# Kernel optimization log

Hardware: AMD Instinct MI355X
Metric: run time of the kernel (lower is better)

The kernel has to match this reference:

```python
import jax, jax.numpy as jnp
import numpy as np

DIMS = [784, 256, 128, 64, 32, 10]
PCT = [0.5, 0.1, 0.5, 0.5]          # KWinners percent_on per layer
KS = [128, 13, 32, 16]              # k = round(n * percent_on)
BOOST = 1.4
SPARSITY = 0.1                      # fraction of weights kept nonzero
BATCH = 65536


def setup_inputs() -> dict:
    key = jax.random.key(0)
    ks = jax.random.split(key, 16)
    inp = {"x": jax.random.normal(ks[0], (BATCH, 784), jnp.float32)}
    for i in range(5):
        fan_in = DIMS[i]
        bound = 1.0 / np.sqrt(fan_in)
        w = jax.random.uniform(ks[1 + 2 * i], (DIMS[i + 1], DIMS[i]), jnp.float32, -bound, bound)
        b = jax.random.uniform(ks[2 + 2 * i], (DIMS[i + 1],), jnp.float32, -bound, bound)
        if i < 4:
            mask = (jax.random.uniform(ks[11 + i], (DIMS[i + 1], DIMS[i])) < SPARSITY).astype(jnp.float32)
            w = w * mask
        inp[f"w{i + 1}"] = w
        inp[f"b{i + 1}"] = b
    for i in range(4):  # duty cycles (buffers driving boosting)
        inp[f"duty{i + 1}"] = jax.random.uniform(
            jax.random.fold_in(key, 100 + i), (DIMS[i + 1],), jnp.float32, 0.0, 2.0 * PCT[i])
    return inp


def kwinners(x, duty, percent_on, k):
    # boost = exp(boost_strength * (target_density - duty_cycle))
    boosted = x * jnp.exp(BOOST * (percent_on - duty))
    # per-row k-th largest boosted value as threshold; winners keep raw x
    thresh = jax.lax.top_k(boosted, k)[0][:, -1:]
    return jnp.where(boosted >= thresh, x, jnp.zeros_like(x))


def reference(x, w1, b1, w2, b2, w3, b3, w4, b4, w5, b5, duty1, duty2, duty3, duty4):
    h = x.reshape(x.shape[0], -1)
    h = kwinners(h @ w1.T + b1, duty1, PCT[0], KS[0])
    h = kwinners(h @ w2.T + b2, duty2, PCT[1], KS[1])
    h = kwinners(h @ w3.T + b3, duty3, PCT[2], KS[2])
    h = kwinners(h @ w4.T + b4, duty4, PCT[3], KS[3])
    return h @ w5.T + b5
```

## Files before the change

kernel.cpp:

```cpp
#include <hip/hip_runtime.h>
#include <cstdint>
#include <cstddef>
#include <math.h>

#define NT 512
#define TROWS 64
#define HS 68

typedef __attribute__((ext_vector_type(8))) short bf16x8;
typedef __attribute__((ext_vector_type(4))) float f32x4;

#define WSP2_OFF 614400
#define WSP3_OFF 712704
#define WSP4_OFF 737280

__device__ __forceinline__ uint32_t f2u(float f) {
  uint32_t b = __float_as_uint(f);
  return (b & 0x80000000u) ? ~b : (b | 0x80000000u);
}

__device__ __forceinline__ unsigned short f2bf(float f) {
  uint32_t u = __float_as_uint(f);
  return (unsigned short)((u + 0x7FFFu + ((u >> 16) & 1u)) >> 16);
}
__device__ __forceinline__ float bf2f(unsigned short h) {
  return __uint_as_float(((uint32_t)h) << 16);
}

__device__ __forceinline__ void gload_lds16(const void* g, void* l) {
  __builtin_amdgcn_global_load_lds(
      (const __attribute__((address_space(1))) unsigned int*)g,
      (__attribute__((address_space(3))) unsigned int*)l, 16, 0, 0);
}

__global__ void prep_w1_kernel(const float* __restrict__ w1,
                               unsigned short* __restrict__ wsp) {
  const int idx = blockIdx.x * 256 + threadIdx.x;
  if (idx >= 256 * 800) return;
  const int col = idx / 800, k = idx % 800;
  const float v = (k < 784) ? w1[col * 784 + k] : 0.0f;
  const unsigned short h = f2bf(v);
  const float r1 = v - bf2f(h);
  const unsigned short m = f2bf(r1);
  const float r2 = r1 - bf2f(m);
  const unsigned short l = f2bf(r2);
  const int c = k >> 5, kin = k & 31, kg = kin >> 3, k8 = kin & 7;
  const int tile = col >> 4, c16 = col & 15;
  const size_t base =
      ((size_t)(c * 3) * 16 + tile) * 512 + (size_t)(kg * 16 + c16) * 8 + k8;
  wsp[base]            = h;
  wsp[base + 16 * 512] = m;
  wsp[base + 32 * 512] = l;
}

__global__ void prep_w2_kernel(const float* __restrict__ w2,
                               unsigned short* __restrict__ wsp) {
  const int idx = blockIdx.x * 256 + threadIdx.x;
  if (idx >= 128 * 256) return;
  const int col = idx / 256, k = idx % 256;
  const float v = w2[col * 256 + k];
  const unsigned short h = f2bf(v);
  const float r1 = v - bf2f(h);
  const unsigned short m = f2bf(r1);
  const float r2 = r1 - bf2f(m);
  const unsigned short l = f2bf(r2);
  const int c2 = k >> 5, kin = k & 31, kg = kin >> 3, k8 = kin & 7;
  const int tile = col >> 4, c16 = col & 15;
  unsigned short* w2p = wsp + WSP2_OFF;
  const size_t base =
      ((size_t)(c2 * 3) * 8 + tile) * 512 + (size_t)(kg * 16 + c16) * 8 + k8;
  w2p[base]            = h;
  w2p[base + 8 * 512]  = m;
  w2p[base + 16 * 512] = l;
}

__global__ void prep_w3_kernel(const float* __restrict__ w3,
                               unsigned short* __restrict__ wsp) {
  const int idx = blockIdx.x * 256 + threadIdx.x;
  if (idx >= 64 * 128) return;
  const int col = idx / 128, k = idx % 128;
  const float v = w3[col * 128 + k];
  const unsigned short h = f2bf(v);
  const float r1 = v - bf2f(h);
  const unsigned short m = f2bf(r1);
  const float r2 = r1 - bf2f(m);
  const unsigned short l = f2bf(r2);
  const int c3 = k >> 5, kin = k & 31, kg = kin >> 3, k8 = kin & 7;
  const int tile = col >> 4, c16 = col & 15;
  unsigned short* w3p = wsp + WSP3_OFF;
  const size_t base =
      ((size_t)(c3 * 3) * 4 + tile) * 512 + (size_t)(kg * 16 + c16) * 8 + k8;
  w3p[base]            = h;
  w3p[base + 4 * 512]  = m;
  w3p[base + 8 * 512]  = l;
}

__global__ void prep_w4_kernel(const float* __restrict__ w4,
                               unsigned short* __restrict__ wsp) {
  const int idx = blockIdx.x * 256 + threadIdx.x;
  if (idx >= 32 * 64) return;
  const int col = idx / 64, k = idx % 64;
  const float v = w4[col * 64 + k];
  const unsigned short h = f2bf(v);
  const float r1 = v - bf2f(h);
  const unsigned short m = f2bf(r1);
  const float r2 = r1 - bf2f(m);
  const unsigned short l = f2bf(r2);
  const int c4 = k >> 5, kin = k & 31, kg = kin >> 3, k8 = kin & 7;
  const int tile = col >> 4, c16 = col & 15;
  unsigned short* w4p = wsp + WSP4_OFF;
  const size_t base =
      ((size_t)(c4 * 3) * 2 + tile) * 512 + (size_t)(kg * 16 + c16) * 8 + k8;
  w4p[base]            = h;
  w4p[base + 2 * 512]  = m;
  w4p[base + 4 * 512]  = l;
}

template<int NCOL, int K>
__device__ __forceinline__ void kwinners_inplace(
    float* __restrict__ ht, const float* __restrict__ duty,
    float pct, int wid, int lane)
{
  constexpr int Q = (NCOL + 63) / 64;
  const bool active = (NCOL >= 64) || (lane < NCOL);
  float Bq[Q];
#pragma unroll
  for (int q = 0; q < Q; ++q) {
    const int col = active ? (lane + 64 * q) : 0;
    const float arg = 1.4f * (pct - duty[col]);
    Bq[q] = (float)exp((double)arg);
  }
#pragma unroll
  for (int g = 0; g < 2; ++g) {
    const int r0 = wid * 8 + g * 4;
    float h[Q][4];
    uint32_t u[Q][4];
#pragma unroll
    for (int q = 0; q < Q; ++q) {
      const int col = active ? (lane + 64 * q) : 0;
      *(float4*)&h[q][0] = *(const float4*)&ht[col * HS + r0];
#pragma unroll
      for (int m = 0; m < 4; ++m)
        u[q][m] = active ? f2u(h[q][m] * Bq[q]) : 0u;
    }
    uint32_t prefix[4] = {0u, 0u, 0u, 0u};
    int done = 0;
    for (int bit = 31; bit >= 0 && done != 15; --bit) {
#pragma unroll
      for (int m = 0; m < 4; ++m) {
        if (done & (1 << m)) continue;
        const uint32_t cand = prefix[m] | (1u << bit);
        int cnt = 0;
#pragma unroll
        for (int q = 0; q < Q; ++q)
          cnt += __popcll(__ballot(u[q][m] >= cand));
        if (cnt >= K) {
          prefix[m] = cand;
          if (cnt == K) done |= (1 << m);
        }
      }
    }
#pragma unroll
    for (int m = 0; m < 4; ++m)
#pragma unroll
      for (int q = 0; q < Q; ++q)
        h[q][m] = (u[q][m] >= prefix[m]) ? h[q][m] : 0.0f;
#pragma unroll
    for (int q = 0; q < Q; ++q) {
      const int col = lane + 64 * q;
      if (active) *(float4*)&ht[col * HS + r0] = *(const float4*)&h[q][0];
    }
  }
}

#define SPLIT3(a8, Ah, Am, Al)                                   \
  _Pragma("unroll")                                              \
  for (int j = 0; j < 8; ++j) {                                  \
    const uint32_t u0 = __float_as_uint(a8[j]);                  \
    Ah[j] = (short)(u0 >> 16);                                   \
    const float r1 = a8[j] - __uint_as_float(u0 & 0xFFFF0000u);  \
    const uint32_t u1 = __float_as_uint(r1);                     \
    Am[j] = (short)(u1 >> 16);                                   \
    const float r2 = r1 - __uint_as_float(u1 & 0xFFFF0000u);     \
    Al[j] = (short)(__float_as_uint(r2) >> 16);                  \
  }

#define MFMA6(ACC, Ah, Am, Al, PB, PSTRIDE)                                  \
  {                                                                          \
    bf16x8 B_ = *(const bf16x8*)(PB);                                        \
    ACC = __builtin_amdgcn_mfma_f32_16x16x32_bf16(Ah, B_, ACC, 0, 0, 0);     \
    ACC = __builtin_amdgcn_mfma_f32_16x16x32_bf16(Am, B_, ACC, 0, 0, 0);     \
    ACC = __builtin_amdgcn_mfma_f32_16x16x32_bf16(Al, B_, ACC, 0, 0, 0);     \
    B_ = *(const bf16x8*)((PB) + (PSTRIDE));                                 \
    ACC = __builtin_amdgcn_mfma_f32_16x16x32_bf16(Ah, B_, ACC, 0, 0, 0);     \
    ACC = __builtin_amdgcn_mfma_f32_16x16x32_bf16(Am, B_, ACC, 0, 0, 0);     \
    B_ = *(const bf16x8*)((PB) + 2 * (PSTRIDE));                             \
    ACC = __builtin_amdgcn_mfma_f32_16x16x32_bf16(Ah, B_, ACC, 0, 0, 0);     \
  }

__global__ __launch_bounds__(NT, 4)
void sparse_fcnet_kernel(
    const float* __restrict__ x,
    const unsigned short* __restrict__ wsp,
    const float* __restrict__ b1, const float* __restrict__ b2,
    const float* __restrict__ b3, const float* __restrict__ b4,
    const float* __restrict__ w5, const float* __restrict__ b5,
    const float* __restrict__ duty1, const float* __restrict__ duty2,
    const float* __restrict__ duty3, const float* __restrict__ duty4,
    float* __restrict__ out)
{
  __shared__ float ht[256 * HS];
  __shared__ float stg[2592];

  const int tid  = threadIdx.x;
  const int lane = tid & 63;
  const int wid  = tid >> 6;
  const int R0   = blockIdx.x * TROWS;

  const int rt  = wid & 3;
  const int ch  = wid >> 2;
  const int l15 = lane & 15;
  const int kg  = lane >> 4;

  {
    unsigned short* wp = (unsigned short*)ht;

    f32x4 acc[8];
#pragma unroll
    for (int t = 0; t < 8; ++t) acc[t] = 0.0f;

    const size_t xrow = (size_t)(R0 + rt * 16 + l15) * 784;
    float xc[8];
    {
      const float4 va = *(const float4*)&x[xrow + kg * 8];
      const float4 vb = *(const float4*)&x[xrow + kg * 8 + 4];
      xc[0]=va.x; xc[1]=va.y; xc[2]=va.z; xc[3]=va.w;
      xc[4]=vb.x; xc[5]=vb.y; xc[6]=vb.z; xc[7]=vb.w;
    }

    for (int c = 0; c < 25; ++c) {
      __syncthreads();
      {
        const unsigned short* wc = wsp + (size_t)c * 24576;
#pragma unroll
        for (int u = 0; u < 6; ++u) {
          const int ubase = (u * 512 + wid * 64) * 8;
          gload_lds16(wc + ubase + lane * 8, &wp[ubase]);
        }
      }
      bf16x8 Ah, Am, Al;
      SPLIT3(xc, Ah, Am, Al)
      if (c < 24) {
        const int kn = (c + 1) * 32 + kg * 8;
        if (kn < 784) {
          const float4 va = *(const float4*)&x[xrow + kn];
          const float4 vb = *(const float4*)&x[xrow + kn + 4];
          xc[0]=va.x; xc[1]=va.y; xc[2]=va.z; xc[3]=va.w;
          xc[4]=vb.x; xc[5]=vb.y; xc[6]=vb.z; xc[7]=vb.w;
        } else {
#pragma unroll
          for (int j = 0; j < 8; ++j) xc[j] = 0.0f;
        }
      }
      __syncthreads();

#pragma unroll
      for (int t = 0; t < 8; ++t) {
        const unsigned short* pb = (const unsigned short*)&wp[(ch * 8 + t) * 512 + lane * 8];
        MFMA6(acc[t], Ah, Am, Al, pb, 8192)
      }
    }
    __syncthreads();

#pragma unroll
    for (int t = 0; t < 8; ++t) {
      const int col_g = ch * 128 + t * 16 + l15;
      const float bv = b1[col_g];
      float4 v = {acc[t].x + bv, acc[t].y + bv, acc[t].z + bv, acc[t].w + bv};
      *(float4*)&ht[col_g * HS + rt * 16 + kg * 4] = v;
    }
  }
  __syncthreads();
  kwinners_inplace<256, 128>(ht, duty1, 0.5f, wid, lane);
  __syncthreads();

  {
    const unsigned short* wsp2 = wsp + WSP2_OFF;
    f32x4 acc2[4];
#pragma unroll
    for (int t = 0; t < 4; ++t) acc2[t] = 0.0f;

    for (int c2 = 0; c2 < 8; ++c2) {
      float a8[8];
#pragma unroll
      for (int j = 0; j < 8; ++j)
        a8[j] = ht[(c2 * 32 + kg * 8 + j) * HS + rt * 16 + l15];
      bf16x8 Ah, Am, Al;
      SPLIT3(a8, Ah, Am, Al)
      const unsigned short* wc2 =
          wsp2 + (size_t)(c2 * 3) * 4096 + (size_t)(ch * 4) * 512 + lane * 8;
#pragma unroll
      for (int t = 0; t < 4; ++t) {
        const unsigned short* pb = wc2 + t * 512;
        MFMA6(acc2[t], Ah, Am, Al, pb, 4096)
      }
    }
    __syncthreads();
#pragma unroll
    for (int t = 0; t < 4; ++t) {
      const int col_g = ch * 64 + t * 16 + l15;
      const float bv = b2[col_g];
      float4 v = {acc2[t].x + bv, acc2[t].y + bv, acc2[t].z + bv, acc2[t].w + bv};
      *(float4*)&ht[col_g * HS + rt * 16 + kg * 4] = v;
    }
  }
  __syncthreads();
  kwinners_inplace<128, 13>(ht, duty2, 0.1f, wid, lane);
  __syncthreads();

  {
    const unsigned short* wsp3 = wsp + WSP3_OFF;
    f32x4 acc3[2];
    acc3[0] = 0.0f; acc3[1] = 0.0f;

    for (int c3 = 0; c3 < 4; ++c3) {
      float a8[8];
#pragma unroll
      for (int j = 0; j < 8; ++j)
        a8[j] = ht[(c3 * 32 + kg * 8 + j) * HS + rt * 16 + l15];
      bf16x8 Ah, Am, Al;
      SPLIT3(a8, Ah, Am, Al)
      const unsigned short* wc3 =
          wsp3 + (size_t)(c3 * 3) * 2048 + (size_t)(ch * 2) * 512 + lane * 8;
#pragma unroll
      for (int t = 0; t < 2; ++t) {
        const unsigned short* pb = wc3 + t * 512;
        MFMA6(acc3[t], Ah, Am, Al, pb, 2048)
      }
    }
    __syncthreads();
#pragma unroll
    for (int t = 0; t < 2; ++t) {
      const int col_g = ch * 32 + t * 16 + l15;
      const float bv = b3[col_g];
      float4 v = {acc3[t].x + bv, acc3[t].y + bv, acc3[t].z + bv, acc3[t].w + bv};
      *(float4*)&ht[col_g * HS + rt * 16 + kg * 4] = v;
    }
  }
  __syncthreads();
  kwinners_inplace<64, 32>(ht, duty3, 0.5f, wid, lane);
  __syncthreads();

  {
    const unsigned short* wsp4 = wsp + WSP4_OFF;
    f32x4 acc4;
    acc4 = 0.0f;

    for (int c4 = 0; c4 < 2; ++c4) {
      float a8[8];
#pragma unroll
      for (int j = 0; j < 8; ++j)
        a8[j] = ht[(c4 * 32 + kg * 8 + j) * HS + rt * 16 + l15];
      bf16x8 Ah, Am, Al;
      SPLIT3(a8, Ah, Am, Al)
      const unsigned short* pb =
          wsp4 + (size_t)(c4 * 3) * 1024 + (size_t)ch * 512 + lane * 8;
      MFMA6(acc4, Ah, Am, Al, pb, 1024)
    }
    __syncthreads();
    {
      const int col_g = ch * 16 + l15;
      const float bv = b4[col_g];
      float4 v = {acc4.x + bv, acc4.y + bv, acc4.z + bv, acc4.w + bv};
      *(float4*)&ht[col_g * HS + rt * 16 + kg * 4] = v;
    }
  }
  __syncthreads();
  kwinners_inplace<32, 16>(ht, duty4, 0.5f, wid, lane);
  __syncthreads();

  {
    if (tid < 320) stg[tid] = w5[tid];
    if (tid < 10)  stg[320 + tid] = b5[tid];
    __syncthreads();
    for (int o = tid; o < 640; o += NT) {
      const int row = o / 10, col = o % 10;
      float acc = 0.0f;
#pragma unroll
      for (int kk = 0; kk < 32; ++kk)
        acc = fmaf(ht[kk * HS + row], stg[col * 32 + kk], acc);
      out[(size_t)(R0 + row) * 10 + col] = acc + stg[320 + col];
    }
  }
}

extern "C" void kernel_launch(void* const* d_in, const int* in_sizes, int n_in,
                              void* d_out, int out_size, void* d_ws, size_t ws_size,
                              hipStream_t stream) {
  const float* x     = (const float*)d_in[0];
  const float* w1    = (const float*)d_in[1];
  const float* b1    = (const float*)d_in[2];
  const float* w2    = (const float*)d_in[3];
  const float* b2    = (const float*)d_in[4];
  const float* w3    = (const float*)d_in[5];
  const float* b3    = (const float*)d_in[6];
  const float* w4    = (const float*)d_in[7];
  const float* b4    = (const float*)d_in[8];
  const float* w5    = (const float*)d_in[9];
  const float* b5    = (const float*)d_in[10];
  const float* duty1 = (const float*)d_in[11];
  const float* duty2 = (const float*)d_in[12];
  const float* duty3 = (const float*)d_in[13];
  const float* duty4 = (const float*)d_in[14];
  float* out = (float*)d_out;
  unsigned short* wsp = (unsigned short*)d_ws;

  hipLaunchKernelGGL(prep_w1_kernel, dim3(800), dim3(256), 0, stream, w1, wsp);
  hipLaunchKernelGGL(prep_w2_kernel, dim3(128), dim3(256), 0, stream, w2, wsp);
  hipLaunchKernelGGL(prep_w3_kernel, dim3(32),  dim3(256), 0, stream, w3, wsp);
  hipLaunchKernelGGL(prep_w4_kernel, dim3(8),   dim3(256), 0, stream, w4, wsp);

  const int rows = in_sizes[0] / 784;
  const int grid = rows / TROWS;
  hipLaunchKernelGGL(sparse_fcnet_kernel, dim3(grid), dim3(NT), 0, stream,
                     x, wsp, b1, b2, b3, b4, w5, b5,
                     duty1, duty2, duty3, duty4, out);
}
```

Baseline: 227.6 us.

## Double-buffer layer-1 weight chunks in LDS and read low-precision part from global

The layer-1 GEMM now prefetches the next weight chunk into a second LDS buffer while computing on the current one. This removes one of the two barriers per chunk iteration. Only the high and mid bf16 weight planes (4 of 6 units) are staged through LDS. The low plane is read directly from global memory, with a register prefetch one tile ahead. This lowers LDS footprint and traffic, but adds global loads inside the MFMA loop and relies on the LDS region being large enough for two 16384-element buffers.

Result: slower. 252.4 us (+10.9%).

```diff
diff --git a/kernel.cpp b/kernel.cpp
--- a/kernel.cpp
+++ b/kernel.cpp
@@ -238,14 +238,25 @@
       xc[4]=vb.x; xc[5]=vb.y; xc[6]=vb.z; xc[7]=vb.w;
     }
 
+    {
+      const unsigned short* wc = wsp;
+#pragma unroll
+      for (int u = 0; u < 4; ++u) {
+        const int ubase = (u * 512 + wid * 64) * 8;
+        gload_lds16(wc + ubase + lane * 8, &wp[ubase]);
+      }
+    }
+    __syncthreads();
+
     for (int c = 0; c < 25; ++c) {
-      __syncthreads();
-      {
-        const unsigned short* wc = wsp + (size_t)c * 24576;
-#pragma unroll
-        for (int u = 0; u < 6; ++u) {
+      unsigned short* cur = wp + (c & 1) * 16384;
+      unsigned short* nxt = wp + ((c + 1) & 1) * 16384;
+      if (c < 24) {
+        const unsigned short* wc = wsp + (size_t)(c + 1) * 24576;
+#pragma unroll
+        for (int u = 0; u < 4; ++u) {
           const int ubase = (u * 512 + wid * 64) * 8;
-          gload_lds16(wc + ubase + lane * 8, &wp[ubase]);
+          gload_lds16(wc + ubase + lane * 8, &nxt[ubase]);
         }
       }
       bf16x8 Ah, Am, Al;
@@ -262,15 +273,28 @@
           for (int j = 0; j < 8; ++j) xc[j] = 0.0f;
         }
       }
+
+      const unsigned short* wl =
+          wsp + (size_t)c * 24576 + 16384 + (size_t)(ch * 8) * 512 + lane * 8;
+      bf16x8 Bl = *(const bf16x8*)(wl);
+
+#pragma unroll
+      for (int t = 0; t < 8; ++t) {
+        bf16x8 Bln;
+        if (t < 7) Bln = *(const bf16x8*)(wl + (t + 1) * 512);
+        const unsigned short* pb = cur + (ch * 8 + t) * 512 + lane * 8;
+        bf16x8 B_ = *(const bf16x8*)(pb);
+        acc[t] = __builtin_amdgcn_mfma_f32_16x16x32_bf16(Ah, B_, acc[t], 0, 0, 0);
+        acc[t] = __builtin_amdgcn_mfma_f32_16x16x32_bf16(Am, B_, acc[t], 0, 0, 0);
+        acc[t] = __builtin_amdgcn_mfma_f32_16x16x32_bf16(Al, B_, acc[t], 0, 0, 0);
+        B_ = *(const bf16x8*)(pb + 8192);
+        acc[t] = __builtin_amdgcn_mfma_f32_16x16x32_bf16(Ah, B_, acc[t], 0, 0, 0);
+        acc[t] = __builtin_amdgcn_mfma_f32_16x16x32_bf16(Am, B_, acc[t], 0, 0, 0);
+        acc[t] = __builtin_amdgcn_mfma_f32_16x16x32_bf16(Ah, Bl, acc[t], 0, 0, 0);
+        if (t < 7) Bl = Bln;
+      }
       __syncthreads();
-
-#pragma unroll
-      for (int t = 0; t < 8; ++t) {
-        const unsigned short* pb = (const unsigned short*)&wp[(ch * 8 + t) * 512 + lane * 8];
-        MFMA6(acc[t], Ah, Am, Al, pb, 8192)
-      }
-    }
-    __syncthreads();
+    }
 
 #pragma unroll
     for (int t = 0; t < 8; ++t) {
```
